# Performance work log

Hardware: AMD Instinct MI355X
Metric: run time of the kernel (lower is better)

## Reference

```python
import jax, jax.numpy as jnp
import numpy as np

SPIN_LEN = 365
TRAIN_LEN = 200000
ML = 2.9086  # mean of second forcing (hard-coded in the torch module)
SL = 1.898   # std of second forcing (hard-coded in the torch module)


def setup_inputs() -> dict:
    key = jax.random.key(0)
    kx, ky, kp = jax.random.split(key, 3)
    B, S = 262144, 1
    x = jax.random.uniform(kx, (B, S, 2), dtype=jnp.float32)
    y_obs = jax.random.uniform(ky, (B, 1), dtype=jnp.float32)
    ks = jax.random.split(kp, 6)
    return {
        "x": x,
        "y_obs": y_obs,
        "epoch": 1,
        "time_lag": 0,
        "weight_r_yom": jax.random.uniform(ks[0], (1, 1), dtype=jnp.float32),
        "weight_r_yom_gw": jax.random.uniform(ks[1], (1, 1), dtype=jnp.float32),
        "weight_r_ylm": jax.random.uniform(ks[2], (1, 1), dtype=jnp.float32),
        "weight_r_yfm": jax.random.uniform(ks[3], (1, 1), dtype=jnp.float32),
        "bias_b0_ylm": jax.random.uniform(ks[4], (1,), dtype=jnp.float32),
        "weight_b2_ylm": jax.random.uniform(ks[5], (1, 1), dtype=jnp.float32),
    }


def reference(x, y_obs, epoch, time_lag, weight_r_yom, weight_r_yom_gw,
              weight_r_ylm, weight_r_yfm, bias_b0_ylm, weight_b2_ylm):
    # x: [B, S, 2] (batch_first). The torch code transposes to [S, B, 2] and
    # runs b-outer / t-inner loops with state threaded across BOTH loops, so
    # the scan order over flattened steps is b-major, t-minor.
    B, S, _ = x.shape
    dt = x.dtype

    # softmax-like mass-balance gate normalization over the 4 scalar weights
    e_om = jnp.exp(weight_r_yom[0, 0])
    e_gw = jnp.exp(weight_r_yom_gw[0, 0])
    e_lm = jnp.exp(weight_r_ylm[0, 0])
    e_fm = jnp.exp(weight_r_yfm[0, 0])
    denom = e_om + e_gw + e_lm + e_fm
    oo = e_om / denom      # constant output gate
    oogw = e_gw / denom    # constant groundwater gate
    ol1 = e_lm / denom     # loss-gate scale
    b0 = bias_b0_ylm[0]
    wb2 = weight_b2_ylm[0, 0]

    # unbiased std, matching torch.std default
    obsstd = jnp.std(y_obs[SPIN_LEN:TRAIN_LEN], ddof=1)

    xv = x[time_lag:]                       # [B', S, 2] (time_lag is static)
    Bp = B - time_lag
    u1 = xv[..., 0].reshape(-1)             # [B'*S] inflow
    u2 = xv[..., 1].reshape(-1)             # [B'*S] loss forcing

    def step(c, u):
        u1_t, u2_t = u
        ol = ol1 * jax.nn.sigmoid(b0 + (u2_t - ML) / SL * wb2)
        f = 1.0 - oo - ol - oogw
        c_new = f * c + u1_t                # ib = 0 -> full inflow enters
        return c_new, (c, ol, f)

    _, (c_prev, ol_s, f_s) = jax.lax.scan(step, jnp.zeros((), dt), (u1, u2))

    # torch stores outputs every t but overwrites; only last t per b survives,
    # using c_0 (state BEFORE that step) and that step's ol/f.
    c0 = c_prev.reshape(Bp, S)[:, -1]
    olL = ol_s.reshape(Bp, S)[:, -1]
    fL = f_s.reshape(Bp, S)[:, -1]

    def pad(v):  # rows b < time_lag stay zero, shape [B, 1]
        return jnp.pad(v, (time_lag, 0))[:, None]

    h_n = pad(oo * c0)          # bp = 0 so h_n == q_n
    c_n = pad(c0)
    l_n = pad(olL * c0)
    gw_n = pad(oogw * c0)
    bp_n = jnp.zeros((B, 1), dt)
    gate_ib = jnp.zeros((B, 1), dt)
    valid = pad(jnp.ones((Bp,), dt))
    gate_oo = oo * valid
    gate_oogw = oogw * valid
    gate_ol = pad(olL)
    gate_f = pad(fL)
    obs_std = obsstd * valid
    h_nout = jnp.concatenate([h_n, obs_std], axis=1)
    return (h_n, c_n, l_n, gw_n, bp_n, gate_ib, gate_oo, gate_oogw,
            gate_ol, gate_f, h_nout, obs_std)
```

## Files before the change

kernel.cpp:

```cpp
#include <hip/hip_runtime.h>
#include <math.h>

#define SPIN 365
#define TRAINL 200000
#define ML 2.9086f
#define SLINV (1.0f / 1.898f)

#define THREADS 512
#define ITEMS 2
#define CHUNK (THREADS * ITEMS)
#define NW (THREADS / 64)

struct Sc { float oo, oogw, ol1, b0, k; };

__device__ __forceinline__ Sc get_sc(const float* w0, const float* w1,
                                     const float* w2, const float* w3,
                                     const float* b0p, const float* wb2p) {
  float e_om = __expf(w0[0]);
  float e_gw = __expf(w1[0]);
  float e_lm = __expf(w2[0]);
  float e_fm = __expf(w3[0]);
  float denom = e_om + e_gw + e_lm + e_fm;
  Sc s;
  s.oo   = e_om / denom;
  s.oogw = e_gw / denom;
  s.ol1  = e_lm / denom;
  s.b0   = b0p[0];
  s.k    = wb2p[0] * SLINV;
  return s;
}

__device__ __forceinline__ float sigm_fast(float z) {
  return __fdividef(1.0f, 1.0f + __expf(-z));
}


extern "C" __global__ __launch_bounds__(THREADS) void kf(
    const float* __restrict__ x, const float* __restrict__ y,
    const int* __restrict__ tlp,
    const float* __restrict__ w0, const float* __restrict__ w1,
    const float* __restrict__ w2, const float* __restrict__ w3,
    const float* __restrict__ b0p, const float* __restrict__ wb2p,
    float* __restrict__ out, float* __restrict__ ws,
    unsigned int* __restrict__ flags, int B, int G)
{
  const int g = blockIdx.x, tid = threadIdx.x;
  const int lane = tid & 63, wid = tid >> 6;
  const int tl = tlp[0];
  const Sc sc = get_sc(w0, w1, w2, w3, b0p, wb2p);
  const int base = g * CHUNK + tid * ITEMS;
  const bool full = (base + ITEMS) <= B;
  const int YB = min(G, (TRAINL + CHUNK - 1) / CHUNK);

  float u1v[ITEMS], u2v[ITEMS];
  if (full) {
    float4 a = *(const float4*)(x + 2 * (size_t)base);
    u1v[0] = a.x; u2v[0] = a.y; u1v[1] = a.z; u2v[1] = a.w;
  } else {
    for (int j = 0; j < ITEMS; j++) {
      int p = base + j;
      u1v[j] = (p < B) ? x[2*(size_t)p]     : 0.f;
      u2v[j] = (p < B) ? x[2*(size_t)p + 1] : 0.f;
    }
  }

  float P = 1.f, Q = 0.f;
  float olv[ITEMS], fv[ITEMS];
  for (int j = 0; j < ITEMS; j++) {
    int p = base + j;
    float ol = sc.ol1 * sigm_fast(sc.b0 + (u2v[j] - ML) * sc.k);
    float f  = 1.0f - sc.oo - ol - sc.oogw;
    olv[j] = ol; fv[j] = f;
    bool act = (p >= tl) && (p < B);
    if (act) { Q = f * Q + u1v[j]; P *= f; }
  }

  float iP = P, iQ = Q;
  #pragma unroll
  for (int off = 1; off < 64; off <<= 1) {
    float pa = __shfl_up(iP, off);
    float pb = __shfl_up(iQ, off);
    if (lane >= off) { iQ = iP * pb + iQ; iP = iP * pa; }
  }

  float s = 0.f, ss = 0.f;
  if (full && base < TRAINL) {
    float2 yv = *(const float2*)(y + base);
    float vv[2] = { yv.x, yv.y };
    for (int j = 0; j < ITEMS; j++) {
      int p = base + j;
      if (p >= SPIN && p < TRAINL) { s += vv[j]; ss += vv[j]*vv[j]; }
    }
  } else {
    for (int j = 0; j < ITEMS; j++) {
      int p = base + j;
      if (p >= SPIN && p < TRAINL && p < B) { float v = y[p]; s += v; ss += v*v; }
    }
  }
  #pragma unroll
  for (int off = 1; off < 64; off <<= 1) {
    s  += __shfl_xor(s,  off);
    ss += __shfl_xor(ss, off);
  }

  __shared__ float wOA[NW], wOB[NW], rS[NW], rSS[NW];
  __shared__ float wAA[NW], wAB[NW], rSY[NW], rSSY[NW];
  __shared__ float shCg;
  if (lane == 63) { wOA[wid] = iP; wOB[wid] = iQ; }
  if (lane == 0)  { rS[wid] = s; rSS[wid] = ss; }
  __syncthreads();

  if (tid == 0) {
    float A = 1.f, Bq = 0.f, S = 0.f, SS = 0.f;
    #pragma unroll
    for (int w = 0; w < NW; w++) {
      Bq = wOA[w] * Bq + wOB[w];
      A  = wOA[w] * A;
      S += rS[w]; SS += rSS[w];
    }
    __hip_atomic_store(&ws[g],       A,  __ATOMIC_RELAXED, __HIP_MEMORY_SCOPE_AGENT);
    __hip_atomic_store(&ws[G + g],   Bq, __ATOMIC_RELAXED, __HIP_MEMORY_SCOPE_AGENT);
    __hip_atomic_store(&ws[2*G + g], S,  __ATOMIC_RELAXED, __HIP_MEMORY_SCOPE_AGENT);
    __hip_atomic_store(&ws[3*G + g], SS, __ATOMIC_RELAXED, __HIP_MEMORY_SCOPE_AGENT);
    asm volatile("s_waitcnt vmcnt(0)" ::: "memory");
    __hip_atomic_store(&flags[g], 1u, __ATOMIC_RELAXED, __HIP_MEMORY_SCOPE_AGENT);
  }

  if (full) {
    bool a0 = (base >= tl), a1 = (base + 1 >= tl);
    *(float2*)(out + 4*(size_t)B + base) = make_float2(0.f, 0.f);
    *(float2*)(out + 5*(size_t)B + base) = make_float2(0.f, 0.f);
    *(float2*)(out + 6*(size_t)B + base) = make_float2(a0?sc.oo:0.f,  a1?sc.oo:0.f);
    *(float2*)(out + 7*(size_t)B + base) = make_float2(a0?sc.oogw:0.f,a1?sc.oogw:0.f);
    *(float2*)(out + 8*(size_t)B + base) = make_float2(a0?olv[0]:0.f, a1?olv[1]:0.f);
    *(float2*)(out + 9*(size_t)B + base) = make_float2(a0?fv[0]:0.f,  a1?fv[1]:0.f);
  } else {
    for (int j = 0; j < ITEMS; j++) {
      int p = base + j;
      if (p < B) {
        bool act = (p >= tl);
        out[4*(size_t)B+p] = 0.f;                  out[5*(size_t)B+p] = 0.f;
        out[6*(size_t)B+p] = act ? sc.oo   : 0.f;  out[7*(size_t)B+p] = act ? sc.oogw : 0.f;
        out[8*(size_t)B+p] = act ? olv[j]  : 0.f;  out[9*(size_t)B+p] = act ? fv[j]   : 0.f;
      }
    }
  }

  float eP = __shfl_up(iP, 1);
  float eQ = __shfl_up(iQ, 1);
  if (lane == 0) { eP = 1.f; eQ = 0.f; }
  float OWA = 1.f, OWB = 0.f;
  for (int w = 0; w < wid; w++) { OWB = wOA[w] * OWB + wOB[w]; OWA *= wOA[w]; }
  const float Ae = eP * OWA;
  const float Be = eP * OWB + eQ;

  const int NEED = (g > YB) ? g : YB;
  if (tid < NEED) {
    bool done = false;
    while (!done) {
      unsigned f = __hip_atomic_load(&flags[tid], __ATOMIC_RELAXED, __HIP_MEMORY_SCOPE_AGENT);
      if (f == 1u) done = true;
      else __builtin_amdgcn_s_sleep(1);
    }
  }
  asm volatile("" ::: "memory");

  float jP = 1.f, jQ = 0.f, ys = 0.f, yss = 0.f;
  if (tid < g) {
    jP = __hip_atomic_load(&ws[tid],     __ATOMIC_RELAXED, __HIP_MEMORY_SCOPE_AGENT);
    jQ = __hip_atomic_load(&ws[G + tid], __ATOMIC_RELAXED, __HIP_MEMORY_SCOPE_AGENT);
  }
  if (tid < YB) {
    ys  = __hip_atomic_load(&ws[2*G + tid], __ATOMIC_RELAXED, __HIP_MEMORY_SCOPE_AGENT);
    yss = __hip_atomic_load(&ws[3*G + tid], __ATOMIC_RELAXED, __HIP_MEMORY_SCOPE_AGENT);
  }

  #pragma unroll
  for (int off = 1; off < 64; off <<= 1) {
    float pa = __shfl_up(jP, off);
    float pb = __shfl_up(jQ, off);
    if (lane >= off) { jQ = jP * pb + jQ; jP = jP * pa; }
  }
  #pragma unroll
  for (int off = 1; off < 64; off <<= 1) {
    ys  += __shfl_xor(ys,  off);
    yss += __shfl_xor(yss, off);
  }
  if (lane == 63) { wAA[wid] = jP; wAB[wid] = jQ; }
  if (lane == 0)  { rSY[wid] = ys; rSSY[wid] = yss; }
  __syncthreads();

  if (g == 0) {
    if (tid == 0) shCg = 0.f;
  } else if (tid == g - 1) {
    float AWB = 0.f, AWA = 1.f;
    for (int w = 0; w < wid; w++) { AWB = wAA[w] * AWB + wAB[w]; AWA *= wAA[w]; }
    shCg = jP * AWB + jQ;
  }

  float S = 0.f, SS = 0.f;
  #pragma unroll
  for (int w = 0; w < NW; w++) { S += rSY[w]; SS += rSSY[w]; }
  float n = (float)(TRAINL - SPIN);
  float mean = S / n;
  float var = (SS - n * mean * mean) / (n - 1.0f);
  float ostd = sqrtf(fmaxf(var, 0.f));
  __syncthreads();
  const float Cg = shCg;

  float c = Ae * Cg + Be;
  float vh[ITEMS], vc[ITEMS], vl[ITEMS], vgw[ITEMS], vos[ITEMS];
  for (int j = 0; j < ITEMS; j++) {
    int p = base + j;
    bool act = (p >= tl) && (p < B);
    float c0 = c;
    vh[j]  = sc.oo * c0;
    vc[j]  = c0;
    vl[j]  = olv[j] * c0;
    vgw[j] = sc.oogw * c0;
    vos[j] = act ? ostd : 0.f;
    if (act) { c = fv[j] * c + u1v[j]; }
  }

  if (full) {
    *(float2*)(out + (size_t)base)        = make_float2(vh[0], vh[1]);
    *(float2*)(out + (size_t)B + base)    = make_float2(vc[0], vc[1]);
    *(float2*)(out + 2*(size_t)B + base)  = make_float2(vl[0], vl[1]);
    *(float2*)(out + 3*(size_t)B + base)  = make_float2(vgw[0], vgw[1]);
    *(float2*)(out + 12*(size_t)B + base) = make_float2(vos[0], vos[1]);
    *(float4*)(out + 10*(size_t)B + 2*(size_t)base) = make_float4(vh[0], vos[0], vh[1], vos[1]);
  } else {
    for (int j = 0; j < ITEMS; j++) {
      int p = base + j;
      if (p < B) {
        out[(size_t)p]            = vh[j];
        out[(size_t)B + p]        = vc[j];
        out[2*(size_t)B + p]      = vl[j];
        out[3*(size_t)B + p]      = vgw[j];
        out[12*(size_t)B + p]     = vos[j];
        out[10*(size_t)B + 2*p]     = vh[j];
        out[10*(size_t)B + 2*p + 1] = vos[j];
      }
    }
  }
}

extern "C" void kernel_launch(void* const* d_in, const int* in_sizes, int n_in,
                              void* d_out, int out_size, void* d_ws, size_t ws_size,
                              hipStream_t stream) {
  const float* x   = (const float*)d_in[0];
  const float* y   = (const float*)d_in[1];
  const int*   tl  = (const int*)d_in[3];
  const float* w0  = (const float*)d_in[4];
  const float* w1  = (const float*)d_in[5];
  const float* w2  = (const float*)d_in[6];
  const float* w3  = (const float*)d_in[7];
  const float* b0  = (const float*)d_in[8];
  const float* wb2 = (const float*)d_in[9];

  float* out = (float*)d_out;
  float* ws  = (float*)d_ws;

  const int B = in_sizes[0] / 2;
  const int G = (B + CHUNK - 1) / CHUNK;

  unsigned int* flags = (unsigned int*)(ws + 4 * (size_t)G);

  kf<<<G, THREADS, 0, stream>>>(x, y, tl, w0, w1, w2, w3, b0, wb2,
                                out, ws, flags, B, G);
}
```

Baseline: 82.88 us.

## Halve block size, single-wave flag polling and serial-then-scan block prefix, nontemporal stores

```diff
diff --git a/kernel.cpp b/kernel.cpp
--- a/kernel.cpp
+++ b/kernel.cpp
@@ -6,10 +6,13 @@
 #define ML 2.9086f
 #define SLINV (1.0f / 1.898f)
 
-#define THREADS 512
+#define THREADS 256
 #define ITEMS 2
 #define CHUNK (THREADS * ITEMS)
 #define NW (THREADS / 64)
+
+typedef float v2f __attribute__((ext_vector_type(2)));
+typedef float v4f __attribute__((ext_vector_type(4)));
 
 struct Sc { float oo, oogw, ol1, b0, k; };
 
@@ -32,6 +35,15 @@
 
 __device__ __forceinline__ float sigm_fast(float z) {
   return __fdividef(1.0f, 1.0f + __expf(-z));
+}
+
+__device__ __forceinline__ void nts2(float* p, float a, float b) {
+  v2f v = { a, b };
+  __builtin_nontemporal_store(v, (v2f*)p);
+}
+__device__ __forceinline__ void nts4(float* p, float a, float b, float c, float d) {
+  v4f v = { a, b, c, d };
+  __builtin_nontemporal_store(v, (v4f*)p);
 }
 
 
@@ -104,8 +116,7 @@
   }
 
   __shared__ float wOA[NW], wOB[NW], rS[NW], rSS[NW];
-  __shared__ float wAA[NW], wAB[NW], rSY[NW], rSSY[NW];
-  __shared__ float shCg;
+  __shared__ float shCg, shS, shSS;
   if (lane == 63) { wOA[wid] = iP; wOB[wid] = iQ; }
   if (lane == 0)  { rS[wid] = s; rSS[wid] = ss; }
   __syncthreads();
@@ -128,12 +139,12 @@
 
   if (full) {
     bool a0 = (base >= tl), a1 = (base + 1 >= tl);
-    *(float2*)(out + 4*(size_t)B + base) = make_float2(0.f, 0.f);
-    *(float2*)(out + 5*(size_t)B + base) = make_float2(0.f, 0.f);
-    *(float2*)(out + 6*(size_t)B + base) = make_float2(a0?sc.oo:0.f,  a1?sc.oo:0.f);
-    *(float2*)(out + 7*(size_t)B + base) = make_float2(a0?sc.oogw:0.f,a1?sc.oogw:0.f);
-    *(float2*)(out + 8*(size_t)B + base) = make_float2(a0?olv[0]:0.f, a1?olv[1]:0.f);
-    *(float2*)(out + 9*(size_t)B + base) = make_float2(a0?fv[0]:0.f,  a1?fv[1]:0.f);
+    nts2(out + 4*(size_t)B + base, 0.f, 0.f);
+    nts2(out + 5*(size_t)B + base, 0.f, 0.f);
+    nts2(out + 6*(size_t)B + base, a0?sc.oo:0.f,   a1?sc.oo:0.f);
+    nts2(out + 7*(size_t)B + base, a0?sc.oogw:0.f, a1?sc.oogw:0.f);
+    nts2(out + 8*(size_t)B + base, a0?olv[0]:0.f,  a1?olv[1]:0.f);
+    nts2(out + 9*(size_t)B + base, a0?fv[0]:0.f,   a1?fv[1]:0.f);
   } else {
     for (int j = 0; j < ITEMS; j++) {
       int p = base + j;
@@ -155,57 +166,72 @@
   const float Be = eP * OWB + eQ;
 
   const int NEED = (g > YB) ? g : YB;
-  if (tid < NEED) {
-    bool done = false;
-    while (!done) {
-      unsigned f = __hip_atomic_load(&flags[tid], __ATOMIC_RELAXED, __HIP_MEMORY_SCOPE_AGENT);
-      if (f == 1u) done = true;
-      else __builtin_amdgcn_s_sleep(1);
-    }
-  }
+  if (wid == 0) {
+    bool ok = false;
+    while (!ok) {
+      bool mine = true;
+      for (int idx = lane; idx < NEED; idx += 64) {
+        unsigned f = __hip_atomic_load(&flags[idx], __ATOMIC_RELAXED, __HIP_MEMORY_SCOPE_AGENT);
+        mine &= (f == 1u);
+      }
+      ok = __all(mine);
+      if (!ok) __builtin_amdgcn_s_sleep(2);
+    }
+  }
+  __syncthreads();
   asm volatile("" ::: "memory");
 
-  float jP = 1.f, jQ = 0.f, ys = 0.f, yss = 0.f;
-  if (tid < g) {
-    jP = __hip_atomic_load(&ws[tid],     __ATOMIC_RELAXED, __HIP_MEMORY_SCOPE_AGENT);
-    jQ = __hip_atomic_load(&ws[G + tid], __ATOMIC_RELAXED, __HIP_MEMORY_SCOPE_AGENT);
-  }
-  if (tid < YB) {
-    ys  = __hip_atomic_load(&ws[2*G + tid], __ATOMIC_RELAXED, __HIP_MEMORY_SCOPE_AGENT);
-    yss = __hip_atomic_load(&ws[3*G + tid], __ATOMIC_RELAXED, __HIP_MEMORY_SCOPE_AGENT);
-  }
-
-  #pragma unroll
-  for (int off = 1; off < 64; off <<= 1) {
-    float pa = __shfl_up(jP, off);
-    float pb = __shfl_up(jQ, off);
-    if (lane >= off) { jQ = jP * pb + jQ; jP = jP * pa; }
-  }
-  #pragma unroll
-  for (int off = 1; off < 64; off <<= 1) {
-    ys  += __shfl_xor(ys,  off);
-    yss += __shfl_xor(yss, off);
-  }
-  if (lane == 63) { wAA[wid] = jP; wAB[wid] = jQ; }
-  if (lane == 0)  { rSY[wid] = ys; rSSY[wid] = yss; }
+  if (wid == 0) {
+    float cA = 1.f, cB = 0.f;
+    float capA = 1.f, capB = 0.f;
+    bool cap = false;
+    #pragma unroll
+    for (int k = 0; k < 8; k++) {
+      int idx = lane * 8 + k;
+      if (idx == g) { capA = cA; capB = cB; cap = true; }
+      if (idx < G) {
+        float aP = __hip_atomic_load(&ws[idx],     __ATOMIC_RELAXED, __HIP_MEMORY_SCOPE_AGENT);
+        float aQ = __hip_atomic_load(&ws[G + idx], __ATOMIC_RELAXED, __HIP_MEMORY_SCOPE_AGENT);
+        cB = aP * cB + aQ;
+        cA = aP * cA;
+      }
+    }
+    float jP = cA, jQ = cB;
+    #pragma unroll
+    for (int off = 1; off < 64; off <<= 1) {
+      float pa = __shfl_up(jP, off);
+      float pb = __shfl_up(jQ, off);
+      if (lane >= off) { jQ = jP * pb + jQ; jP = jP * pa; }
+    }
+    float exQ = __shfl_up(jQ, 1);
+    float exP = __shfl_up(jP, 1);
+    if (lane == 0) { exQ = 0.f; exP = 1.f; }
+    (void)exP;
+    if (cap) shCg = capA * exQ + capB;
+  }
+  if (wid == 1) {
+    float S = 0.f, SS = 0.f;
+    #pragma unroll
+    for (int k = 0; k < 8; k++) {
+      int idx = lane * 8 + k;
+      if (idx < YB) {
+        S  += __hip_atomic_load(&ws[2*G + idx], __ATOMIC_RELAXED, __HIP_MEMORY_SCOPE_AGENT);
+        SS += __hip_atomic_load(&ws[3*G + idx], __ATOMIC_RELAXED, __HIP_MEMORY_SCOPE_AGENT);
+      }
+    }
+    #pragma unroll
+    for (int off = 1; off < 64; off <<= 1) {
+      S  += __shfl_xor(S,  off);
+      SS += __shfl_xor(SS, off);
+    }
+    if (lane == 0) { shS = S; shSS = SS; }
+  }
   __syncthreads();
 
-  if (g == 0) {
-    if (tid == 0) shCg = 0.f;
-  } else if (tid == g - 1) {
-    float AWB = 0.f, AWA = 1.f;
-    for (int w = 0; w < wid; w++) { AWB = wAA[w] * AWB + wAB[w]; AWA *= wAA[w]; }
-    shCg = jP * AWB + jQ;
-  }
-
-  float S = 0.f, SS = 0.f;
-  #pragma unroll
-  for (int w = 0; w < NW; w++) { S += rSY[w]; SS += rSSY[w]; }
-  float n = (float)(TRAINL - SPIN);
-  float mean = S / n;
-  float var = (SS - n * mean * mean) / (n - 1.0f);
+  float nY = (float)(TRAINL - SPIN);
+  float mean = shS / nY;
+  float var = (shSS - nY * mean * mean) / (nY - 1.0f);
   float ostd = sqrtf(fmaxf(var, 0.f));
-  __syncthreads();
   const float Cg = shCg;
 
   float c = Ae * Cg + Be;
@@ -223,12 +249,12 @@
   }
 
   if (full) {
-    *(float2*)(out + (size_t)base)        = make_float2(vh[0], vh[1]);
-    *(float2*)(out + (size_t)B + base)    = make_float2(vc[0], vc[1]);
-    *(float2*)(out + 2*(size_t)B + base)  = make_float2(vl[0], vl[1]);
-    *(float2*)(out + 3*(size_t)B + base)  = make_float2(vgw[0], vgw[1]);
-    *(float2*)(out + 12*(size_t)B + base) = make_float2(vos[0], vos[1]);
-    *(float4*)(out + 10*(size_t)B + 2*(size_t)base) = make_float4(vh[0], vos[0], vh[1], vos[1]);
+    nts2(out + (size_t)base,        vh[0],  vh[1]);
+    nts2(out + (size_t)B + base,    vc[0],  vc[1]);
+    nts2(out + 2*(size_t)B + base,  vl[0],  vl[1]);
+    nts2(out + 3*(size_t)B + base,  vgw[0], vgw[1]);
+    nts2(out + 12*(size_t)B + base, vos[0], vos[1]);
+    nts4(out + 10*(size_t)B + 2*(size_t)base, vh[0], vos[0], vh[1], vos[1]);
   } else {
     for (int j = 0; j < ITEMS; j++) {
       int p = base + j;
```

Result: no change. 83.43 us (+0.7%).
